# Performance work log

Hardware: AMD Instinct MI355X
Metric: run time of the kernel (lower is better)

Reference implementation:

```python
import jax, jax.numpy as jnp
import numpy as np

K, H, W, SIGMA = 21, 64, 64, 2
B = 256


def _build_heatmaps():
    # Faithful vectorized version of the module's precomputed table:
    # heatmaps[mu_x, mu_y, y, x] = exp(-((x-mu_x)^2 + (y-mu_y)^2) / (2*sigma^2))
    # truncated to the window |x-mu_x| <= 6*sigma, |y-mu_y| <= 6*sigma, else 0.
    tmp = SIGMA * 6
    xs = np.arange(W, dtype=np.float32)
    ys = np.arange(H, dtype=np.float32)
    dx = xs[None, :] - xs[:, None]  # (mu_x, x)
    dy = ys[None, :] - ys[:, None]  # (mu_y, y)
    g = np.exp(-(dx[:, None, None, :] ** 2 + dy[None, :, :, None] ** 2) / (2.0 * SIGMA ** 2))
    mask = (np.abs(dx)[:, None, None, :] <= tmp) & (np.abs(dy)[None, :, :, None] <= tmp)
    return (g * mask).astype(np.float32)  # (W, H, H, W)


def setup_inputs() -> dict:
    key = jax.random.key(0)
    y = jax.random.normal(key, (B, K, H, W), dtype=jnp.float32)
    heatmaps = jnp.asarray(_build_heatmaps())
    false_matrix = 1.0 - jnp.eye(K, dtype=jnp.float32)
    return {"y": y, "heatmaps": heatmaps, "false_matrix": false_matrix}


def reference(y, heatmaps, false_matrix):
    b, k, h, w = y.shape
    y = jax.lax.stop_gradient(y)  # original detaches y
    flat = y.reshape(b, k, h * w)
    idx = jnp.argmax(flat, axis=2)          # (B, K)
    maxvals = jnp.max(flat, axis=2)         # (B, K)
    px = idx % w                            # x coordinate
    py = idx // w                           # y coordinate
    valid = maxvals > 0.0                   # pred_mask zeroes coords when max <= 0
    px = jnp.where(valid, px, 0)
    py = jnp.where(valid, py, 0)
    ground_truth = heatmaps[px, py]         # gather -> (B, K, H, W)
    # ground_false[b, j] = clip(sum_k gt[b, k] * false_matrix[k, j], 0, 1)
    ground_false = jnp.clip(
        jnp.einsum('bkhw,kj->bjhw', ground_truth, false_matrix), 0.0, 1.0)
    return ground_truth, ground_false
```

## Files before the change

kernel.cpp:

```cpp
#include <hip/hip_runtime.h>

#define BB 256
#define KK 21
#define HH 64
#define WW 64
#define HW 4096
#define TMP 12
#define INV2S2 0.125f

typedef float f32x4 __attribute__((ext_vector_type(4)));

__device__ __forceinline__ void amax_merge(float& bv, int& bi, float v, int i)
{
    if (v > bv || (v == bv && i < bi)) { bv = v; bi = i; }
}

__device__ __forceinline__ float clip01(float x)
{
    return fminf(fmaxf(x, 0.0f), 1.0f);
}

__global__ __launch_bounds__(256) void pl_argmax_kernel(
    const float* __restrict__ y, int* __restrict__ coords)
{
    const int row = blockIdx.x;
    const f32x4* __restrict__ p4 =
        reinterpret_cast<const f32x4*>(y + (size_t)row * HW);
    const int tid = threadIdx.x;

    float best = -INFINITY;
    int bidx = 0x7fffffff;

    #pragma unroll
    for (int c = 0; c < 4; ++c) {
        const int q = c * 256 + tid;
        const f32x4 v = p4[q];
        const int base = q << 2;
        amax_merge(best, bidx, v.x, base + 0);
        amax_merge(best, bidx, v.y, base + 1);
        amax_merge(best, bidx, v.z, base + 2);
        amax_merge(best, bidx, v.w, base + 3);
    }

    #pragma unroll
    for (int off = 32; off > 0; off >>= 1) {
        const float ov = __shfl_down(best, off);
        const int   oi = __shfl_down(bidx, off);
        amax_merge(best, bidx, ov, oi);
    }

    __shared__ float sv[4];
    __shared__ int   si[4];
    const int wave = tid >> 6;
    if ((tid & 63) == 0) { sv[wave] = best; si[wave] = bidx; }
    __syncthreads();

    if (tid == 0) {
        #pragma unroll
        for (int w = 1; w < 4; ++w)
            amax_merge(best, bidx, sv[w], si[w]);
        int px = bidx & (WW - 1);
        int py = bidx >> 6;
        if (!(best > 0.0f)) { px = 0; py = 0; }
        coords[row] = px | (py << 8);
    }
}

__global__ __launch_bounds__(256) void pl_expand_kernel(
    const int* __restrict__ coords,
    f32x4* __restrict__ gt4, f32x4* __restrict__ gf4)
{
    const int b   = blockIdx.x >> 2;
    const int p4i = ((blockIdx.x & 3) << 8) | threadIdx.x;
    const int tid = threadIdx.x;

    __shared__ __align__(16) float sEx[KK * 64];
    __shared__ float sEy[KK * 64];

    for (int i = tid; i < KK * 64; i += 256) {
        const int k  = i >> 6;
        const int c  = i & 63;
        const int pk = coords[b * KK + k];
        const int px = pk & 0xff;
        const int py = pk >> 8;
        const int dx = c - px;
        const int dy = c - py;
        sEx[i] = (dx >= -TMP && dx <= TMP) ? __expf(-(float)(dx * dx) * INV2S2) : 0.0f;
        sEy[i] = (dy >= -TMP && dy <= TMP) ? __expf(-(float)(dy * dy) * INV2S2) : 0.0f;
    }
    __syncthreads();

    const int yy = p4i >> 4;
    const int xq = p4i & 15;
    const f32x4* __restrict__ sEx4 = reinterpret_cast<const f32x4*>(sEx);
    const size_t base = ((size_t)b * KK) << 10;

    f32x4 S = (f32x4)(0.0f);
    #pragma unroll
    for (int k = 0; k < KK; ++k) {
        const float ey = sEy[(k << 6) + yy];
        const f32x4 ex = sEx4[(k << 4) + xq];
        const f32x4 v  = ex * ey;
        __builtin_nontemporal_store(v, &gt4[base + (k << 10) + p4i]);
        S += v;
    }

    #pragma unroll
    for (int k = 0; k < KK; ++k) {
        const float ey = sEy[(k << 6) + yy];
        const f32x4 ex = sEx4[(k << 4) + xq];
        const f32x4 v  = ex * ey;
        f32x4 o;
        o.x = clip01(S.x - v.x);
        o.y = clip01(S.y - v.y);
        o.z = clip01(S.z - v.z);
        o.w = clip01(S.w - v.w);
        __builtin_nontemporal_store(o, &gf4[base + (k << 10) + p4i]);
    }
}

extern "C" void kernel_launch(void* const* d_in, const int* in_sizes, int n_in,
                              void* d_out, int out_size, void* d_ws, size_t ws_size,
                              hipStream_t stream)
{
    const float* y = (const float*)d_in[0];

    float* gt = (float*)d_out;
    float* gf = gt + (size_t)BB * KK * HW;
    int* coords = (int*)d_ws;

    pl_argmax_kernel<<<BB * KK, 256, 0, stream>>>(y, coords);
    pl_expand_kernel<<<BB * 4, 256, 0, stream>>>(
        coords, (f32x4*)gt, (f32x4*)gf);
}
```

Before: 51.95 us.

## Fuse ground-truth writes into argmax kernel and split gf kernel by channel halves

The argmax kernel now computes each row's separable Gaussian in shared memory and writes its ground-truth heatmap directly, so the ground-truth stores happen alongside the input reads. The second kernel only writes ground_false. It uses twice as many blocks, with each thread handling half of the K channels after recomputing the full sum. This moves half the output traffic into the bandwidth-light argmax phase and raises parallelism in the second kernel, at the cost of computing the sum redundantly in each thread half.

Result: faster. 46.94 us (-9.6%).

```diff
diff --git a/kernel.cpp b/kernel.cpp
--- a/kernel.cpp
+++ b/kernel.cpp
@@ -20,8 +20,9 @@
     return fminf(fmaxf(x, 0.0f), 1.0f);
 }
 
-__global__ __launch_bounds__(256) void pl_argmax_kernel(
-    const float* __restrict__ y, int* __restrict__ coords)
+__global__ __launch_bounds__(256) void pl_argmax_gt_kernel(
+    const float* __restrict__ y, int* __restrict__ coords,
+    f32x4* __restrict__ gt4)
 {
     const int row = blockIdx.x;
     const f32x4* __restrict__ p4 =
@@ -51,6 +52,10 @@
 
     __shared__ float sv[4];
     __shared__ int   si[4];
+    __shared__ int   scoord;
+    __shared__ __align__(16) float sEx[64];
+    __shared__ float sEy[64];
+
     const int wave = tid >> 6;
     if ((tid & 63) == 0) { sv[wave] = best; si[wave] = bidx; }
     __syncthreads();
@@ -63,16 +68,43 @@
         int py = bidx >> 6;
         if (!(best > 0.0f)) { px = 0; py = 0; }
         coords[row] = px | (py << 8);
+        scoord = px | (py << 8);
+    }
+    __syncthreads();
+
+    if (tid < 128) {
+        const int c  = tid & 63;
+        const int pk = scoord;
+        if (tid < 64) {
+            const int dx = c - (pk & 0xff);
+            sEx[c] = (dx >= -TMP && dx <= TMP)
+                   ? __expf(-(float)(dx * dx) * INV2S2) : 0.0f;
+        } else {
+            const int dy = c - (pk >> 8);
+            sEy[c] = (dy >= -TMP && dy <= TMP)
+                   ? __expf(-(float)(dy * dy) * INV2S2) : 0.0f;
+        }
+    }
+    __syncthreads();
+
+    const f32x4* __restrict__ sEx4 = reinterpret_cast<const f32x4*>(sEx);
+    const size_t obase = ((size_t)row) << 10;
+    #pragma unroll
+    for (int c = 0; c < 4; ++c) {
+        const int q  = c * 256 + tid;
+        const int yy = q >> 4;
+        const int xq = q & 15;
+        const f32x4 v = sEx4[xq] * sEy[yy];
+        __builtin_nontemporal_store(v, &gt4[obase + q]);
     }
 }
 
-__global__ __launch_bounds__(256) void pl_expand_kernel(
-    const int* __restrict__ coords,
-    f32x4* __restrict__ gt4, f32x4* __restrict__ gf4)
+__global__ __launch_bounds__(256) void pl_gf_kernel(
+    const int* __restrict__ coords, f32x4* __restrict__ gf4)
 {
-    const int b   = blockIdx.x >> 2;
-    const int p4i = ((blockIdx.x & 3) << 8) | threadIdx.x;
-    const int tid = threadIdx.x;
+    const int b      = blockIdx.x >> 3;
+    const int eighth = blockIdx.x & 7;
+    const int tid    = threadIdx.x;
 
     __shared__ __align__(16) float sEx[KK * 64];
     __shared__ float sEy[KK * 64];
@@ -90,32 +122,42 @@
     }
     __syncthreads();
 
-    const int yy = p4i >> 4;
-    const int xq = p4i & 15;
+    const int sub   = tid & 127;
+    const int khalf = tid >> 7;
+    const int p4i   = (eighth << 7) | sub;
+    const int yy    = p4i >> 4;
+    const int xq    = p4i & 15;
     const f32x4* __restrict__ sEx4 = reinterpret_cast<const f32x4*>(sEx);
-    const size_t base = ((size_t)b * KK) << 10;
 
     f32x4 S = (f32x4)(0.0f);
     #pragma unroll
-    for (int k = 0; k < KK; ++k) {
-        const float ey = sEy[(k << 6) + yy];
-        const f32x4 ex = sEx4[(k << 4) + xq];
-        const f32x4 v  = ex * ey;
-        __builtin_nontemporal_store(v, &gt4[base + (k << 10) + p4i]);
-        S += v;
-    }
+    for (int k = 0; k < KK; ++k)
+        S += sEx4[(k << 4) + xq] * sEy[(k << 6) + yy];
 
-    #pragma unroll
-    for (int k = 0; k < KK; ++k) {
-        const float ey = sEy[(k << 6) + yy];
-        const f32x4 ex = sEx4[(k << 4) + xq];
-        const f32x4 v  = ex * ey;
-        f32x4 o;
-        o.x = clip01(S.x - v.x);
-        o.y = clip01(S.y - v.y);
-        o.z = clip01(S.z - v.z);
-        o.w = clip01(S.w - v.w);
-        __builtin_nontemporal_store(o, &gf4[base + (k << 10) + p4i]);
+    const size_t base = ((size_t)b * KK) << 10;
+
+    if (khalf == 0) {
+        #pragma unroll
+        for (int k = 0; k < 11; ++k) {
+            const f32x4 v = sEx4[(k << 4) + xq] * sEy[(k << 6) + yy];
+            f32x4 o;
+            o.x = clip01(S.x - v.x);
+            o.y = clip01(S.y - v.y);
+            o.z = clip01(S.z - v.z);
+            o.w = clip01(S.w - v.w);
+            __builtin_nontemporal_store(o, &gf4[base + (k << 10) + p4i]);
+        }
+    } else {
+        #pragma unroll
+        for (int k = 11; k < KK; ++k) {
+            const f32x4 v = sEx4[(k << 4) + xq] * sEy[(k << 6) + yy];
+            f32x4 o;
+            o.x = clip01(S.x - v.x);
+            o.y = clip01(S.y - v.y);
+            o.z = clip01(S.z - v.z);
+            o.w = clip01(S.w - v.w);
+            __builtin_nontemporal_store(o, &gf4[base + (k << 10) + p4i]);
+        }
     }
 }
 
@@ -129,7 +171,6 @@
     float* gf = gt + (size_t)BB * KK * HW;
     int* coords = (int*)d_ws;
 
-    pl_argmax_kernel<<<BB * KK, 256, 0, stream>>>(y, coords);
-    pl_expand_kernel<<<BB * 4, 256, 0, stream>>>(
-        coords, (f32x4*)gt, (f32x4*)gf);
+    pl_argmax_gt_kernel<<<BB * KK, 256, 0, stream>>>(y, coords, (f32x4*)gt);
+    pl_gf_kernel<<<BB * 8, 256, 0, stream>>>(coords, (f32x4*)gf);
 }
```
